# Optimization experiments

Hardware: AMD Instinct MI355X
Metric: run time of the kernel (lower is better)

The kernel has to match this reference:

```python
import jax, jax.numpy as jnp
import numpy as np

B, N, E = 32, 128, 8192
IMG, LOC, H = 2048, 5, 128


def setup_inputs() -> dict:
    key = jax.random.key(0)
    ks = jax.random.split(key, 10)
    img_feat = jax.random.normal(ks[0], (B, N, IMG), dtype=jnp.float32)
    img_loc = jax.random.uniform(ks[1], (B, N, LOC), dtype=jnp.float32)
    edge_src = jax.random.randint(ks[2], (E,), 0, N, dtype=jnp.int32)
    edge_dst = jax.random.randint(ks[3], (E,), 0, N, dtype=jnp.int32)
    # learned parameters (nn.Linear: y = x @ W + b)
    W_img = jax.random.normal(ks[4], (IMG, H), dtype=jnp.float32) / np.sqrt(IMG)
    b_img = jnp.zeros((H,), dtype=jnp.float32)
    W_loc = jax.random.normal(ks[5], (LOC, H), dtype=jnp.float32) / np.sqrt(LOC)
    b_loc = jnp.zeros((H,), dtype=jnp.float32)
    W_rel = jax.random.normal(ks[6], (2 * H, H), dtype=jnp.float32) / np.sqrt(2 * H)
    b_rel = jnp.zeros((H,), dtype=jnp.float32)
    return {
        "img_feat": img_feat, "img_loc": img_loc,
        "edge_src": edge_src, "edge_dst": edge_dst,
        "W_img": W_img, "b_img": b_img,
        "W_loc": W_loc, "b_loc": b_loc,
        "W_rel": W_rel, "b_rel": b_rel,
    }


def reference(img_feat, img_loc, edge_src, edge_dst,
              W_img, b_img, W_loc, b_loc, W_rel, b_rel):
    # img_fc / img_loc_fc projections
    img = jnp.einsum('bni,ih->bnh', img_feat, W_img) + b_img      # [B,N,H]
    loc = jnp.einsum('bnl,lh->bnh', img_loc, W_loc) + b_loc       # [B,N,H]
    node_feat = img + loc                                          # [B,N,H]
    # per-edge gather + concat + linear (batched over all edges at once;
    # split W_rel to avoid materializing the concat)
    src_f = jnp.take(img, edge_src, axis=1)                        # [B,E,H]
    dst_f = jnp.take(img, edge_dst, axis=1)                        # [B,E,H]
    edge_feat = (jnp.einsum('beh,hk->bek', src_f, W_rel[:H]) +
                 jnp.einsum('beh,hk->bek', dst_f, W_rel[H:]) + b_rel)  # [B,E,H]
    return node_feat, edge_feat
```

## Files before the change

### kernel.cpp

```cpp
#include <hip/hip_runtime.h>
#include <hip/hip_bf16.h>
#include <stdint.h>

#define B_   32
#define N_   128
#define E_   8192
#define IMG_ 2048
#define H_   128

typedef __attribute__((ext_vector_type(8))) short bf16x8;
typedef __attribute__((ext_vector_type(4))) float f32x4;

__device__ inline uint16_t f2bf(float x) {
    uint32_t u = __float_as_uint(x);
    uint32_t r = (u + 0x7FFFu + ((u >> 16) & 1u)) >> 16;
    return (uint16_t)r;
}
__device__ inline float bf2f(short x) {
    return __uint_as_float(((uint32_t)(uint16_t)x) << 16);
}

__global__ void prep_kernel(const float* __restrict__ W_img,
                            const float* __restrict__ W_rel,
                            uint16_t* __restrict__ Wt_img,
                            uint16_t* __restrict__ Wt_rel) {
    int tid = blockIdx.x * blockDim.x + threadIdx.x;
    if (tid < IMG_ * H_) {
        int c = tid / IMG_, k = tid % IMG_;
        Wt_img[tid] = f2bf(W_img[k * H_ + c]);
    } else {
        int t2 = tid - IMG_ * H_;
        if (t2 < 2 * H_ * H_) {
            int c = t2 / 256, k = t2 % 256;
            Wt_rel[t2] = f2bf(W_rel[k * H_ + c]);
        }
    }
}

__global__ __launch_bounds__(1024) void node_proj_kernel(
    const float* __restrict__ img_feat,
    const uint16_t* __restrict__ Wt_img,
    const uint16_t* __restrict__ Wt_rel,
    const float* __restrict__ img_loc,
    const float* __restrict__ b_img,
    const float* __restrict__ W_loc,
    const float* __restrict__ b_loc,
    const float* __restrict__ b_rel,
    float* __restrict__ out_node,
    uint16_t* __restrict__ proj) {
    __shared__ __align__(16) char lds_raw[131072];
    float (*red)[16][128] = (float (*)[16][128])lds_raw;
    uint16_t (*imgb)[136] = (uint16_t (*)[136])lds_raw;

    int strip = blockIdx.x;
    int w  = threadIdx.x >> 6;
    int l  = threadIdx.x & 63;
    int lr = l & 15;
    int kq = l >> 4;
    int kl = kq * 8;

    const float* arow = img_feat + (size_t)(strip * 16 + lr) * IMG_;
    f32x4 acc[8];
    #pragma unroll
    for (int n = 0; n < 8; n++) acc[n] = (f32x4){0.f, 0.f, 0.f, 0.f};
    int k0 = w * 128;
    #pragma unroll
    for (int ks = 0; ks < 4; ks++) {
        int k = k0 + ks * 32 + kl;
        float4 a0 = *(const float4*)(arow + k);
        float4 a1 = *(const float4*)(arow + k + 4);
        bf16x8 af;
        af[0] = (short)f2bf(a0.x); af[1] = (short)f2bf(a0.y);
        af[2] = (short)f2bf(a0.z); af[3] = (short)f2bf(a0.w);
        af[4] = (short)f2bf(a1.x); af[5] = (short)f2bf(a1.y);
        af[6] = (short)f2bf(a1.z); af[7] = (short)f2bf(a1.w);
        #pragma unroll
        for (int n = 0; n < 8; n++) {
            bf16x8 bf = *(const bf16x8*)(Wt_img + (size_t)(n * 16 + lr) * IMG_ + k);
            acc[n] = __builtin_amdgcn_mfma_f32_16x16x32_bf16(af, bf, acc[n], 0, 0, 0);
        }
    }

    #pragma unroll
    for (int n = 0; n < 8; n++)
        #pragma unroll
        for (int r = 0; r < 4; r++)
            red[w][kq * 4 + r][n * 16 + lr] = acc[n][r];
    __syncthreads();

    int tid  = threadIdx.x;
    int row0 = tid >> 7, col = tid & 127;
    int row1 = row0 + 8;
    float s0 = 0.f, s1 = 0.f;
    #pragma unroll
    for (int ww = 0; ww < 16; ww++) {
        s0 += red[ww][row0][col];
        s1 += red[ww][row1][col];
    }
    __syncthreads();

    {
        float bi = b_img[col];
        float bl = b_loc[col];
        float wl[5];
        #pragma unroll
        for (int j = 0; j < 5; j++) wl[j] = W_loc[j * H_ + col];

        float img0 = s0 + bi, img1 = s1 + bi;
        int g0 = strip * 16 + row0, g1 = strip * 16 + row1;
        const float* lc0 = img_loc + g0 * 5;
        const float* lc1 = img_loc + g1 * 5;
        float loc0 = bl, loc1 = bl;
        #pragma unroll
        for (int j = 0; j < 5; j++) { loc0 += lc0[j] * wl[j]; loc1 += lc1[j] * wl[j]; }
        out_node[(size_t)g0 * H_ + col] = img0 + loc0;
        out_node[(size_t)g1 * H_ + col] = img1 + loc1;
        imgb[row0][col] = f2bf(img0);
        imgb[row1][col] = f2bf(img1);
    }
    __syncthreads();

    int cp = w * 16 + lr;
    const uint16_t* bbase = (cp < 128)
        ? (Wt_rel + (size_t)cp * 256)
        : (Wt_rel + (size_t)(cp - 128) * 256 + 128);
    f32x4 pacc = (f32x4){0.f, 0.f, 0.f, 0.f};
    #pragma unroll
    for (int ks = 0; ks < 4; ks++) {
        int k = ks * 32 + kl;
        bf16x8 af = *(const bf16x8*)(&imgb[lr][k]);
        bf16x8 bf = *(const bf16x8*)(bbase + k);
        pacc = __builtin_amdgcn_mfma_f32_16x16x32_bf16(af, bf, pacc, 0, 0, 0);
    }
    float brel = (cp < 128) ? b_rel[cp] : 0.f;
    #pragma unroll
    for (int r = 0; r < 4; r++) {
        int grow = strip * 16 + kq * 4 + r;
        proj[(size_t)grow * 256 + cp] = f2bf(pacc[r] + brel);
    }
}

__global__ __launch_bounds__(256) void edge_kernel(
    const uint16_t* __restrict__ proj,
    const int* __restrict__ edge_src,
    const int* __restrict__ edge_dst,
    float* __restrict__ out_edge) {
    int t = blockIdx.x * 256 + threadIdx.x;
    #pragma unroll
    for (int it = 0; it < 8; it++) {
        int g = t + it * 524288;
        int b = g >> 17;
        int r = g & 131071;
        int e = r >> 4;
        int c = (r & 15) * 8;
        int s = edge_src[e];
        int d = edge_dst[e];
        bf16x8 a  = *(const bf16x8*)(proj + (((size_t)b * N_ + s) * 256 + c));
        bf16x8 bb = *(const bf16x8*)(proj + (((size_t)b * N_ + d) * 256 + 128 + c));
        float* op = out_edge + ((size_t)b * E_ + e) * (size_t)H_ + c;
        float4 o0, o1;
        o0.x = bf2f(a[0]) + bf2f(bb[0]);
        o0.y = bf2f(a[1]) + bf2f(bb[1]);
        o0.z = bf2f(a[2]) + bf2f(bb[2]);
        o0.w = bf2f(a[3]) + bf2f(bb[3]);
        o1.x = bf2f(a[4]) + bf2f(bb[4]);
        o1.y = bf2f(a[5]) + bf2f(bb[5]);
        o1.z = bf2f(a[6]) + bf2f(bb[6]);
        o1.w = bf2f(a[7]) + bf2f(bb[7]);
        *(float4*)op = o0;
        *(float4*)(op + 4) = o1;
    }
}

extern "C" void kernel_launch(void* const* d_in, const int* in_sizes, int n_in,
                              void* d_out, int out_size, void* d_ws, size_t ws_size,
                              hipStream_t stream) {
    const float* img_feat = (const float*)d_in[0];
    const float* img_loc  = (const float*)d_in[1];
    const int*   edge_src = (const int*)d_in[2];
    const int*   edge_dst = (const int*)d_in[3];
    const float* W_img    = (const float*)d_in[4];
    const float* b_img    = (const float*)d_in[5];
    const float* W_loc    = (const float*)d_in[6];
    const float* b_loc    = (const float*)d_in[7];
    const float* W_rel    = (const float*)d_in[8];
    const float* b_rel    = (const float*)d_in[9];

    float* out_node = (float*)d_out;
    float* out_edge = out_node + (size_t)B_ * N_ * H_;

    char* ws = (char*)d_ws;
    uint16_t* Wt_img = (uint16_t*)ws;
    uint16_t* Wt_rel = (uint16_t*)(ws + 524288);
    uint16_t* proj   = (uint16_t*)(ws + 524288 + 65536);

    prep_kernel<<<dim3((IMG_ * H_ + 2 * H_ * H_) / 256), dim3(256), 0, stream>>>(
        W_img, W_rel, Wt_img, Wt_rel);

    node_proj_kernel<<<dim3(256), dim3(1024), 0, stream>>>(
        img_feat, Wt_img, Wt_rel, img_loc, b_img, W_loc, b_loc, b_rel,
        out_node, proj);

    edge_kernel<<<dim3(2048), dim3(256), 0, stream>>>(
        proj, edge_src, edge_dst, out_edge);
}
```

Baseline: 58.00 us.

## Stage A strip via async global-to-LDS loads, prefetch B fragments, tile-transpose prep

The node projection kernel now copies the whole 16x2048 fp32 activation strip into LDS with global_load_lds, using an XOR swizzle against bank conflicts, before the MFMA loop. The Wt_img fragments are loaded one k-step ahead into registers so global latency overlaps the MFMAs. The prep kernel transposes W_img through a padded shared tile so reads are coalesced, instead of using strided per-element reads. This costs more registers and an extra barrier, and the whole 128KB LDS buffer now serves as the staging area.

Result: no change. 58.02 us (+0.0%).

```diff
diff --git a/kernel.cpp b/kernel.cpp
--- a/kernel.cpp
+++ b/kernel.cpp
@@ -20,20 +20,28 @@
     return __uint_as_float(((uint32_t)(uint16_t)x) << 16);
 }
 
-__global__ void prep_kernel(const float* __restrict__ W_img,
-                            const float* __restrict__ W_rel,
-                            uint16_t* __restrict__ Wt_img,
-                            uint16_t* __restrict__ Wt_rel) {
-    int tid = blockIdx.x * blockDim.x + threadIdx.x;
-    if (tid < IMG_ * H_) {
-        int c = tid / IMG_, k = tid % IMG_;
-        Wt_img[tid] = f2bf(W_img[k * H_ + c]);
+__global__ __launch_bounds__(256) void prep_kernel(
+    const float* __restrict__ W_img, const float* __restrict__ W_rel,
+    uint16_t* __restrict__ Wt_img, uint16_t* __restrict__ Wt_rel) {
+    int bid = blockIdx.x, tid = threadIdx.x;
+    if (bid < 32) {
+        __shared__ float t[64][129];
+        int k0 = bid * 64;
+        const float* src = W_img + (size_t)k0 * H_;
+        #pragma unroll
+        for (int it = 0; it < 32; it++) {
+            int idx = it * 256 + tid;
+            t[idx >> 7][idx & 127] = src[idx];
+        }
+        __syncthreads();
+        int c = tid >> 1, kh = (tid & 1) * 32;
+        uint16_t* dst = Wt_img + (size_t)c * IMG_ + k0 + kh;
+        #pragma unroll
+        for (int j = 0; j < 32; j++) dst[j] = f2bf(t[kh + j][c]);
     } else {
-        int t2 = tid - IMG_ * H_;
-        if (t2 < 2 * H_ * H_) {
-            int c = t2 / 256, k = t2 % 256;
-            Wt_rel[t2] = f2bf(W_rel[k * H_ + c]);
-        }
+        int t2 = (bid - 32) * 256 + tid;
+        int c = t2 >> 8, k = t2 & 255;
+        Wt_rel[t2] = f2bf(W_rel[k * H_ + c]);
     }
 }
 
@@ -53,33 +61,62 @@
     uint16_t (*imgb)[136] = (uint16_t (*)[136])lds_raw;
 
     int strip = blockIdx.x;
-    int w  = threadIdx.x >> 6;
-    int l  = threadIdx.x & 63;
+    int tid = threadIdx.x;
+    int w  = tid >> 6;
+    int l  = tid & 63;
     int lr = l & 15;
     int kq = l >> 4;
-    int kl = kq * 8;
-
-    const float* arow = img_feat + (size_t)(strip * 16 + lr) * IMG_;
+
+    const char* gA = (const char*)(img_feat + (size_t)strip * 16 * IMG_);
+    #pragma unroll
+    for (int r = 0; r < 8; r++) {
+        int L = r * 16384 + tid * 16;
+        int row = L >> 13;
+        int koff = L & 8191;
+        int gsrc = row * 8192 + (koff ^ ((row & 7) << 4));
+        __builtin_amdgcn_global_load_lds(
+            (const __attribute__((address_space(1))) void*)(gA + gsrc),
+            (__attribute__((address_space(3))) void*)(lds_raw + L), 16, 0, 0);
+    }
+
+    int kbase = w * 128 + kq * 8;
+    bf16x8 bcur[8];
+    #pragma unroll
+    for (int n = 0; n < 8; n++)
+        bcur[n] = *(const bf16x8*)(Wt_img + (size_t)(n * 16 + lr) * IMG_ + kbase);
+
+    __syncthreads();
+
     f32x4 acc[8];
     #pragma unroll
     for (int n = 0; n < 8; n++) acc[n] = (f32x4){0.f, 0.f, 0.f, 0.f};
-    int k0 = w * 128;
+    int sw = (lr & 7) << 4;
     #pragma unroll
     for (int ks = 0; ks < 4; ks++) {
-        int k = k0 + ks * 32 + kl;
-        float4 a0 = *(const float4*)(arow + k);
-        float4 a1 = *(const float4*)(arow + k + 4);
+        int koffb = w * 512 + ks * 128 + kq * 32;
+        float4 a0 = *(const float4*)(lds_raw + (size_t)lr * 8192 + (koffb ^ sw));
+        float4 a1 = *(const float4*)(lds_raw + (size_t)lr * 8192 + ((koffb + 16) ^ sw));
+        bf16x8 bn[8];
+        if (ks < 3) {
+            int kn = kbase + (ks + 1) * 32;
+            #pragma unroll
+            for (int n = 0; n < 8; n++)
+                bn[n] = *(const bf16x8*)(Wt_img + (size_t)(n * 16 + lr) * IMG_ + kn);
+        }
         bf16x8 af;
         af[0] = (short)f2bf(a0.x); af[1] = (short)f2bf(a0.y);
         af[2] = (short)f2bf(a0.z); af[3] = (short)f2bf(a0.w);
         af[4] = (short)f2bf(a1.x); af[5] = (short)f2bf(a1.y);
         af[6] = (short)f2bf(a1.z); af[7] = (short)f2bf(a1.w);
         #pragma unroll
-        for (int n = 0; n < 8; n++) {
-            bf16x8 bf = *(const bf16x8*)(Wt_img + (size_t)(n * 16 + lr) * IMG_ + k);
-            acc[n] = __builtin_amdgcn_mfma_f32_16x16x32_bf16(af, bf, acc[n], 0, 0, 0);
+        for (int n = 0; n < 8; n++)
+            acc[n] = __builtin_amdgcn_mfma_f32_16x16x32_bf16(af, bcur[n], acc[n], 0, 0, 0);
+        if (ks < 3) {
+            #pragma unroll
+            for (int n = 0; n < 8; n++) bcur[n] = bn[n];
         }
     }
+    __syncthreads();
 
     #pragma unroll
     for (int n = 0; n < 8; n++)
@@ -88,7 +125,6 @@
             red[w][kq * 4 + r][n * 16 + lr] = acc[n][r];
     __syncthreads();
 
-    int tid  = threadIdx.x;
     int row0 = tid >> 7, col = tid & 127;
     int row1 = row0 + 8;
     float s0 = 0.f, s1 = 0.f;
@@ -105,7 +141,6 @@
         float wl[5];
         #pragma unroll
         for (int j = 0; j < 5; j++) wl[j] = W_loc[j * H_ + col];
-
         float img0 = s0 + bi, img1 = s1 + bi;
         int g0 = strip * 16 + row0, g1 = strip * 16 + row1;
         const float* lc0 = img_loc + g0 * 5;
@@ -120,6 +155,7 @@
     }
     __syncthreads();
 
+    int kl = kq * 8;
     int cp = w * 16 + lr;
     const uint16_t* bbase = (cp < 128)
         ? (Wt_rel + (size_t)cp * 256)
@@ -194,8 +230,7 @@
     uint16_t* Wt_rel = (uint16_t*)(ws + 524288);
     uint16_t* proj   = (uint16_t*)(ws + 524288 + 65536);
 
-    prep_kernel<<<dim3((IMG_ * H_ + 2 * H_ * H_) / 256), dim3(256), 0, stream>>>(
-        W_img, W_rel, Wt_img, Wt_rel);
+    prep_kernel<<<dim3(160), dim3(256), 0, stream>>>(W_img, W_rel, Wt_img, Wt_rel);
 
     node_proj_kernel<<<dim3(256), dim3(1024), 0, stream>>>(
         img_feat, Wt_img, Wt_rel, img_loc, b_img, W_loc, b_loc, b_rel,
```
